# Kernel optimization log

Measured on AMD Instinct MI355X. Metric: run time of the kernel, lower is better.

The kernel has to match this reference:

```python
import jax, jax.numpy as jnp
import numpy as np

B, S, H = 64, 1024, 512
NEG = -1e10


def setup_inputs() -> dict:
    key = jax.random.key(0)
    ks = jax.random.split(key, 10)
    hidden = jax.random.normal(ks[0], (B, H), dtype=jnp.float32)
    encoder_outputs = jax.random.normal(ks[1], (S, B, H), dtype=jnp.float32)
    attn_mask = jax.random.randint(ks[2], (B, S), 0, 2, dtype=jnp.int32)
    src_gps_seqs = jax.random.uniform(ks[3], (S, B, 2), dtype=jnp.float32)
    src = jax.random.uniform(ks[4], (S, B, 3), dtype=jnp.float32)
    src_rids = jax.random.randint(ks[5], (S, B, 1), 0, 10000, dtype=jnp.int64)
    input_id = jax.random.randint(ks[6], (B, 1), 0, 10000, dtype=jnp.int64)
    trg_gps_seqs = jax.random.uniform(ks[7], (B, 2), dtype=jnp.float32)
    # learned params: attn = Linear(2H -> H), v = Linear(H -> 1, no bias)
    bound = 1.0 / np.sqrt(2 * H)
    attn_w = jax.random.uniform(ks[8], (H, 2 * H), minval=-bound, maxval=bound, dtype=jnp.float32)
    attn_b = jnp.zeros((H,), dtype=jnp.float32)
    v_w = jax.random.uniform(ks[9], (1, H), minval=-1.0 / np.sqrt(H), maxval=1.0 / np.sqrt(H), dtype=jnp.float32)
    return {"t": 0, "hidden": hidden, "encoder_outputs": encoder_outputs,
            "attn_mask": attn_mask, "src_gps_seqs": src_gps_seqs, "src": src,
            "src_rids": src_rids, "input_id": input_id, "trg_gps_seqs": trg_gps_seqs,
            "attn_w": attn_w, "attn_b": attn_b, "v_w": v_w}


def reference(t, hidden, encoder_outputs, attn_mask, src_gps_seqs, src,
              src_rids, input_id, trg_gps_seqs, attn_w, attn_b, v_w):
    # encoder_outputs: [S, B, H] -> [B, S, H]
    enc = jnp.transpose(encoder_outputs, (1, 0, 2))
    s_len = enc.shape[1]
    # hidden [B, H] broadcast over src_len -> [B, S, H]
    h = jnp.broadcast_to(hidden[:, None, :], (hidden.shape[0], s_len, hidden.shape[1]))
    cat = jnp.concatenate([h, enc], axis=2)                      # [B, S, 2H]
    energy = jnp.tanh(jnp.einsum('bsk,hk->bsh', cat, attn_w) + attn_b)  # [B, S, H]
    attention = jnp.einsum('bsh,oh->bs', energy, v_w)            # [B, S]
    attention = jnp.where(attn_mask == 0, jnp.float32(NEG), attention)
    return jax.nn.softmax(attention, axis=1)
```

## Files before the change

### kernel.cpp

```cpp
#include <hip/hip_runtime.h>
#include <hip/hip_bf16.h>

typedef unsigned short ushort_t;
typedef unsigned int uint_t;
typedef __attribute__((ext_vector_type(8))) short short8;
typedef __attribute__((ext_vector_type(4))) float f32x4;

#define NEG_VAL -1e10f

#define GL16(gp, lp) __builtin_amdgcn_global_load_lds( \
    (const __attribute__((address_space(1))) uint_t*)(gp), \
    (__attribute__((address_space(3))) uint_t*)(lp), 16, 0, 0)

__device__ __forceinline__ ushort_t f2bf(float x) {
    uint_t u = __float_as_uint(x);
    uint_t r = (u + 0x7fffu + ((u >> 16) & 1u)) >> 16;
    return (ushort_t)r;
}

__device__ __forceinline__ uint_t pkbf(float a, float b) {
    return (uint_t)f2bf(a) | ((uint_t)f2bf(b) << 16);
}

__device__ __forceinline__ uint_t cvtpk(float a, float b) {
    uint_t r;
    asm("v_cvt_pk_bf16_f32 %0, %1, %2" : "=v"(r) : "v"(a), "v"(b));
    return r;
}

__device__ __forceinline__ float tanh_fast(float x) {
    float e = __expf(2.0f * x);
    return 1.0f - 2.0f / (e + 1.0f);
}

__global__ void w2conv_kernel(const float* __restrict__ attn_w, ushort_t* __restrict__ w2) {
    int gid = blockIdx.x * 256 + threadIdx.x;
    int h = gid >> 7, q = gid & 127;
    float4 v = *(const float4*)(attn_w + (size_t)h * 1024 + 512 + q * 4);
    uint2 p;
    p.x = pkbf(v.x, v.y);
    p.y = pkbf(v.z, v.w);
    *(uint2*)(w2 + h * 512 + q * 4) = p;
}

__global__ void hproj_kernel(const float* __restrict__ hidden,
                             const float* __restrict__ attn_w,
                             const float* __restrict__ attn_b,
                             float* __restrict__ hb) {
    int gid = blockIdx.x * 256 + threadIdx.x;
    int b = gid >> 9, h = gid & 511;
    const float4* hp = (const float4*)(hidden + (size_t)b * 512);
    const float4* wp = (const float4*)(attn_w + (size_t)h * 1024);
    float a0 = 0.f, a1 = 0.f, a2 = 0.f, a3 = 0.f;
    #pragma unroll 4
    for (int i = 0; i < 128; i += 4) {
        float4 x0 = hp[i + 0], w0 = wp[i + 0];
        a0 += x0.x * w0.x + x0.y * w0.y + x0.z * w0.z + x0.w * w0.w;
        float4 x1 = hp[i + 1], w1 = wp[i + 1];
        a1 += x1.x * w1.x + x1.y * w1.y + x1.z * w1.z + x1.w * w1.w;
        float4 x2 = hp[i + 2], w2v = wp[i + 2];
        a2 += x2.x * w2v.x + x2.y * w2v.y + x2.z * w2v.z + x2.w * w2v.w;
        float4 x3 = hp[i + 3], w3 = wp[i + 3];
        a3 += x3.x * w3.x + x3.y * w3.y + x3.z * w3.z + x3.w * w3.w;
    }
    hb[gid] = attn_b[h] + ((a0 + a1) + (a2 + a3));
}

__global__ __launch_bounds__(256, 2) void gemm_kernel(
    const float* __restrict__ enc,
    const ushort_t* __restrict__ w2,
    const float* __restrict__ hb,
    const float* __restrict__ vw,
    float* __restrict__ part)
{
    __shared__ __align__(16) float As[2][128 * 32];
    __shared__ __align__(16) ushort_t Bs[2][256 * 32];
    __shared__ float red[2][128];

    const int tid = threadIdx.x;
    const int bid = blockIdx.x;
    const int xcd = bid & 7, j = bid >> 3;
    const int mt = xcd * 64 + (j >> 1), nt = j & 1;
    const size_t m0 = (size_t)mt * 128;
    const int h0 = nt * 256;

    const int wv = tid >> 6, l = tid & 63;
    const int wm = wv >> 1, wn = wv & 1;
    const int lr = l & 15, lq = l >> 4;

    const float* aG[4];
    uint_t aL[4];
    #pragma unroll
    for (int i = 0; i < 4; i++) {
        int rowA = i * 32 + wv * 8 + (l >> 3);
        int jA = (l & 7) ^ (l >> 3);
        aG[i] = enc + (m0 + rowA) * 512 + jA * 4;
        aL[i] = (uint_t)(i * 256 + wv * 64) * 16;
    }
    const ushort_t* bG[4];
    uint_t bL[4];
    #pragma unroll
    for (int i = 0; i < 4; i++) {
        int rowB = i * 64 + wv * 16 + (l >> 2);
        int jB = (l & 3) ^ ((l >> 3) & 3);
        bG[i] = w2 + (size_t)(h0 + rowB) * 512 + jB * 8;
        bL[i] = (uint_t)(i * 256 + wv * 64) * 16;
    }

    uint_t aoffL[4], aoffH[4], boff[8];
    #pragma unroll
    for (int mf = 0; mf < 4; mf++) {
        int row = wm * 64 + mf * 16 + lr;
        aoffL[mf] = (uint_t)row * 128 + (uint_t)(((lq * 2 + 0) ^ (row & 7)) * 16);
        aoffH[mf] = (uint_t)row * 128 + (uint_t)(((lq * 2 + 1) ^ (row & 7)) * 16);
    }
    #pragma unroll
    for (int nf = 0; nf < 8; nf++) {
        int r = wn * 128 + nf * 16 + lr;
        boff[nf] = (uint_t)r * 64 + (uint_t)((lq ^ ((r >> 1) & 3)) * 16);
    }

    #define STAGE(kt, buf) do { \
        _Pragma("unroll") \
        for (int i = 0; i < 4; i++) GL16(aG[i] + (kt) * 32, (char*)(&As[(buf)][0]) + aL[i]); \
        _Pragma("unroll") \
        for (int i = 0; i < 4; i++) GL16(bG[i] + (kt) * 32, (char*)(&Bs[(buf)][0]) + bL[i]); \
    } while (0)

    STAGE(0, 0);
    __syncthreads();

    f32x4 acc[4][8] = {};

    #pragma unroll 2
    for (int kt = 0; kt < 16; ++kt) {
        const int cur = kt & 1;
        if (kt < 15) STAGE(kt + 1, cur ^ 1);
        short8 af[4], bfr[8];
        #pragma unroll
        for (int nf = 0; nf < 8; nf++)
            bfr[nf] = *(const short8*)((const char*)(&Bs[cur][0]) + boff[nf]);
        #pragma unroll
        for (int mf = 0; mf < 4; mf++) {
            f32x4 lo = *(const f32x4*)((const char*)(&As[cur][0]) + aoffL[mf]);
            f32x4 hi = *(const f32x4*)((const char*)(&As[cur][0]) + aoffH[mf]);
            union { short8 s; uint_t u[4]; } t;
            t.u[0] = cvtpk(lo[0], lo[1]);
            t.u[1] = cvtpk(lo[2], lo[3]);
            t.u[2] = cvtpk(hi[0], hi[1]);
            t.u[3] = cvtpk(hi[2], hi[3]);
            af[mf] = t.s;
        }
        #pragma unroll
        for (int mf = 0; mf < 4; mf++)
            #pragma unroll
            for (int nf = 0; nf < 8; nf++)
                acc[mf][nf] = __builtin_amdgcn_mfma_f32_16x16x32_bf16(af[mf], bfr[nf], acc[mf][nf], 0, 0, 0);
        __syncthreads();
    }
    #undef STAGE

    float vv[8];
    #pragma unroll
    for (int nf = 0; nf < 8; nf++) vv[nf] = vw[h0 + wn * 128 + nf * 16 + lr];

    #pragma unroll
    for (int mf = 0; mf < 4; mf++) {
        #pragma unroll
        for (int r = 0; r < 4; r++) {
            int row = wm * 64 + mf * 16 + lq * 4 + r;
            int b = row & 63;
            const float* hbp = hb + b * 512 + h0 + wn * 128 + lr;
            float p = 0.f;
            #pragma unroll
            for (int nf = 0; nf < 8; nf++) {
                float x = acc[mf][nf][r] + hbp[nf * 16];
                p += tanh_fast(x) * vv[nf];
            }
            p += __shfl_xor(p, 1);
            p += __shfl_xor(p, 2);
            p += __shfl_xor(p, 4);
            p += __shfl_xor(p, 8);
            if (lr == 0) red[wn][row] = p;
        }
    }
    __syncthreads();
    if (tid < 128) {
        part[(size_t)nt * 65536 + m0 + tid] = red[0][tid] + red[1][tid];
    }
}

__global__ void softmax_kernel(const float* __restrict__ part,
                               const int* __restrict__ mask,
                               float* __restrict__ out) {
    __shared__ float sred[8];
    int b = blockIdx.x;
    int t = threadIdx.x;
    float vals[4];
    float mx = -INFINITY;
    #pragma unroll
    for (int i = 0; i < 4; i++) {
        int s = t + i * 256;
        int row = s * 64 + b;
        float x = part[row] + part[65536 + row];
        if (mask[b * 1024 + s] == 0) x = NEG_VAL;
        vals[i] = x;
        mx = fmaxf(mx, x);
    }
    #pragma unroll
    for (int o = 32; o; o >>= 1) mx = fmaxf(mx, __shfl_xor(mx, o));
    int w = t >> 6;
    if ((t & 63) == 0) sred[w] = mx;
    __syncthreads();
    mx = fmaxf(fmaxf(sred[0], sred[1]), fmaxf(sred[2], sred[3]));
    float sum = 0.f;
    #pragma unroll
    for (int i = 0; i < 4; i++) {
        vals[i] = __expf(vals[i] - mx);
        sum += vals[i];
    }
    #pragma unroll
    for (int o = 32; o; o >>= 1) sum += __shfl_xor(sum, o);
    if ((t & 63) == 0) sred[4 + w] = sum;
    __syncthreads();
    float tot = (sred[4] + sred[5]) + (sred[6] + sred[7]);
    float inv = 1.0f / tot;
    #pragma unroll
    for (int i = 0; i < 4; i++) out[b * 1024 + t + i * 256] = vals[i] * inv;
}

extern "C" void kernel_launch(void* const* d_in, const int* in_sizes, int n_in,
                              void* d_out, int out_size, void* d_ws, size_t ws_size,
                              hipStream_t stream) {
    const float* hidden = (const float*)d_in[1];
    const float* enc    = (const float*)d_in[2];
    const int*   mask   = (const int*)d_in[3];
    const float* attn_w = (const float*)d_in[9];
    const float* attn_b = (const float*)d_in[10];
    const float* vw     = (const float*)d_in[11];
    float* out = (float*)d_out;

    char* ws = (char*)d_ws;
    ushort_t* w2 = (ushort_t*)ws;
    float* hb   = (float*)(ws + 512 * 1024);
    float* part = (float*)(ws + 640 * 1024);

    w2conv_kernel<<<256, 256, 0, stream>>>(attn_w, w2);
    hproj_kernel<<<128, 256, 0, stream>>>(hidden, attn_w, attn_b, hb);
    gemm_kernel<<<1024, 256, 0, stream>>>(enc, w2, hb, vw, part);
    softmax_kernel<<<64, 256, 0, stream>>>(part, mask, out);
}
```

Measured before the change: 95.51 us.

## Enlarge GEMM tile to 256x256 with 512 threads and triple-buffered LDS pipeline

The encoder GEMM block grows to 256 rows and 8 waves, with a 2x4 wave grid. LDS moves to three-stage buffering, using explicit vmcnt waits and raw barriers instead of a full syncthreads per k-step. A and B staging are interleaved with split MFMA halves under raised wave priority. The aim is better latency hiding and more reuse of the B tile, at the cost of about 150 KB LDS per block, which limits occupancy to one block per CU.

```diff
diff --git a/kernel.cpp b/kernel.cpp
--- a/kernel.cpp
+++ b/kernel.cpp
@@ -66,84 +66,94 @@
     hb[gid] = attn_b[h] + ((a0 + a1) + (a2 + a3));
 }
 
-__global__ __launch_bounds__(256, 2) void gemm_kernel(
+__global__ __launch_bounds__(512, 2) void gemm_kernel(
     const float* __restrict__ enc,
     const ushort_t* __restrict__ w2,
     const float* __restrict__ hb,
     const float* __restrict__ vw,
     float* __restrict__ part)
 {
-    __shared__ __align__(16) float As[2][128 * 32];
-    __shared__ __align__(16) ushort_t Bs[2][256 * 32];
-    __shared__ float red[2][128];
+    __shared__ __align__(16) float As[3][256 * 32];
+    __shared__ __align__(16) ushort_t Bs[3][256 * 32];
+    __shared__ float red[4][256];
 
     const int tid = threadIdx.x;
     const int bid = blockIdx.x;
     const int xcd = bid & 7, j = bid >> 3;
-    const int mt = xcd * 64 + (j >> 1), nt = j & 1;
-    const size_t m0 = (size_t)mt * 128;
+    const int mt = xcd * 32 + (j >> 1), nt = j & 1;
+    const size_t m0 = (size_t)mt * 256;
     const int h0 = nt * 256;
 
     const int wv = tid >> 6, l = tid & 63;
-    const int wm = wv >> 1, wn = wv & 1;
+    const int wm = wv >> 2, wn = wv & 3;
     const int lr = l & 15, lq = l >> 4;
 
     const float* aG[4];
     uint_t aL[4];
     #pragma unroll
     for (int i = 0; i < 4; i++) {
-        int rowA = i * 32 + wv * 8 + (l >> 3);
-        int jA = (l & 7) ^ (l >> 3);
-        aG[i] = enc + (m0 + rowA) * 512 + jA * 4;
-        aL[i] = (uint_t)(i * 256 + wv * 64) * 16;
-    }
-    const ushort_t* bG[4];
-    uint_t bL[4];
-    #pragma unroll
-    for (int i = 0; i < 4; i++) {
-        int rowB = i * 64 + wv * 16 + (l >> 2);
-        int jB = (l & 3) ^ ((l >> 3) & 3);
-        bG[i] = w2 + (size_t)(h0 + rowB) * 512 + jB * 8;
-        bL[i] = (uint_t)(i * 256 + wv * 64) * 16;
-    }
-
-    uint_t aoffL[4], aoffH[4], boff[8];
-    #pragma unroll
-    for (int mf = 0; mf < 4; mf++) {
-        int row = wm * 64 + mf * 16 + lr;
-        aoffL[mf] = (uint_t)row * 128 + (uint_t)(((lq * 2 + 0) ^ (row & 7)) * 16);
-        aoffH[mf] = (uint_t)row * 128 + (uint_t)(((lq * 2 + 1) ^ (row & 7)) * 16);
-    }
-    #pragma unroll
-    for (int nf = 0; nf < 8; nf++) {
-        int r = wn * 128 + nf * 16 + lr;
+        int row = i * 64 + (tid >> 3);
+        int jj = (tid & 7) ^ ((tid >> 3) & 7);
+        aG[i] = enc + (m0 + row) * 512 + jj * 4;
+        aL[i] = (uint_t)(i * 512 + wv * 64) * 16;
+    }
+    const ushort_t* bG[2];
+    uint_t bL[2];
+    #pragma unroll
+    for (int i = 0; i < 2; i++) {
+        int row = i * 128 + (tid >> 2);
+        int jj = (tid & 3) ^ ((tid >> 3) & 3);
+        bG[i] = w2 + (size_t)(h0 + row) * 512 + jj * 8;
+        bL[i] = (uint_t)(i * 512 + wv * 64) * 16;
+    }
+
+    uint_t aoff0[8], aoff1[8], boff[4];
+    #pragma unroll
+    for (int mf = 0; mf < 8; mf++) {
+        int r = wm * 128 + mf * 16 + lr;
+        aoff0[mf] = (uint_t)r * 128 + (uint_t)(((lq * 2 + 0) ^ (r & 7)) * 16);
+        aoff1[mf] = (uint_t)r * 128 + (uint_t)(((lq * 2 + 1) ^ (r & 7)) * 16);
+    }
+    #pragma unroll
+    for (int nf = 0; nf < 4; nf++) {
+        int r = wn * 64 + nf * 16 + lr;
         boff[nf] = (uint_t)r * 64 + (uint_t)((lq ^ ((r >> 1) & 3)) * 16);
     }
 
-    #define STAGE(kt, buf) do { \
+    #define STAGE_A(kt, buf) do { \
         _Pragma("unroll") \
         for (int i = 0; i < 4; i++) GL16(aG[i] + (kt) * 32, (char*)(&As[(buf)][0]) + aL[i]); \
+    } while (0)
+    #define STAGE_B(kt, buf) do { \
         _Pragma("unroll") \
-        for (int i = 0; i < 4; i++) GL16(bG[i] + (kt) * 32, (char*)(&Bs[(buf)][0]) + bL[i]); \
+        for (int i = 0; i < 2; i++) GL16(bG[i] + (kt) * 32, (char*)(&Bs[(buf)][0]) + bL[i]); \
     } while (0)
 
-    STAGE(0, 0);
-    __syncthreads();
-
-    f32x4 acc[4][8] = {};
-
-    #pragma unroll 2
+    STAGE_A(0, 0); STAGE_B(0, 0);
+    STAGE_A(1, 1); STAGE_B(1, 1);
+
+    f32x4 acc[8][4] = {};
+
+    #pragma unroll
     for (int kt = 0; kt < 16; ++kt) {
-        const int cur = kt & 1;
-        if (kt < 15) STAGE(kt + 1, cur ^ 1);
-        short8 af[4], bfr[8];
-        #pragma unroll
-        for (int nf = 0; nf < 8; nf++)
+        const int cur = kt % 3;
+        if (kt < 15) { asm volatile("s_waitcnt vmcnt(6)" ::: "memory"); }
+        else         { asm volatile("s_waitcnt vmcnt(0)" ::: "memory"); }
+        __builtin_amdgcn_s_barrier();
+        asm volatile("" ::: "memory");
+
+        if (kt + 2 <= 15) STAGE_A(kt + 2, (kt + 2) % 3);
+
+        short8 bfr[4];
+        #pragma unroll
+        for (int nf = 0; nf < 4; nf++)
             bfr[nf] = *(const short8*)((const char*)(&Bs[cur][0]) + boff[nf]);
+
+        short8 af[4];
         #pragma unroll
         for (int mf = 0; mf < 4; mf++) {
-            f32x4 lo = *(const f32x4*)((const char*)(&As[cur][0]) + aoffL[mf]);
-            f32x4 hi = *(const f32x4*)((const char*)(&As[cur][0]) + aoffH[mf]);
+            f32x4 lo = *(const f32x4*)((const char*)(&As[cur][0]) + aoff0[mf]);
+            f32x4 hi = *(const f32x4*)((const char*)(&As[cur][0]) + aoff1[mf]);
             union { short8 s; uint_t u[4]; } t;
             t.u[0] = cvtpk(lo[0], lo[1]);
             t.u[1] = cvtpk(lo[2], lo[3]);
@@ -151,29 +161,53 @@
             t.u[3] = cvtpk(hi[2], hi[3]);
             af[mf] = t.s;
         }
+        __builtin_amdgcn_s_setprio(1);
         #pragma unroll
         for (int mf = 0; mf < 4; mf++)
             #pragma unroll
-            for (int nf = 0; nf < 8; nf++)
+            for (int nf = 0; nf < 4; nf++)
                 acc[mf][nf] = __builtin_amdgcn_mfma_f32_16x16x32_bf16(af[mf], bfr[nf], acc[mf][nf], 0, 0, 0);
-        __syncthreads();
-    }
-    #undef STAGE
-
-    float vv[8];
-    #pragma unroll
-    for (int nf = 0; nf < 8; nf++) vv[nf] = vw[h0 + wn * 128 + nf * 16 + lr];
-
-    #pragma unroll
-    for (int mf = 0; mf < 4; mf++) {
+        __builtin_amdgcn_s_setprio(0);
+
+        if (kt + 2 <= 15) STAGE_B(kt + 2, (kt + 2) % 3);
+
+        short8 ag[4];
+        #pragma unroll
+        for (int mf = 0; mf < 4; mf++) {
+            f32x4 lo = *(const f32x4*)((const char*)(&As[cur][0]) + aoff0[mf + 4]);
+            f32x4 hi = *(const f32x4*)((const char*)(&As[cur][0]) + aoff1[mf + 4]);
+            union { short8 s; uint_t u[4]; } t;
+            t.u[0] = cvtpk(lo[0], lo[1]);
+            t.u[1] = cvtpk(lo[2], lo[3]);
+            t.u[2] = cvtpk(hi[0], hi[1]);
+            t.u[3] = cvtpk(hi[2], hi[3]);
+            ag[mf] = t.s;
+        }
+        __builtin_amdgcn_s_setprio(1);
+        #pragma unroll
+        for (int mf = 0; mf < 4; mf++)
+            #pragma unroll
+            for (int nf = 0; nf < 4; nf++)
+                acc[mf + 4][nf] = __builtin_amdgcn_mfma_f32_16x16x32_bf16(ag[mf], bfr[nf], acc[mf + 4][nf], 0, 0, 0);
+        __builtin_amdgcn_s_setprio(0);
+    }
+    #undef STAGE_A
+    #undef STAGE_B
+
+    float vv[4];
+    #pragma unroll
+    for (int nf = 0; nf < 4; nf++) vv[nf] = vw[h0 + wn * 64 + nf * 16 + lr];
+
+    #pragma unroll
+    for (int mf = 0; mf < 8; mf++) {
         #pragma unroll
         for (int r = 0; r < 4; r++) {
-            int row = wm * 64 + mf * 16 + lq * 4 + r;
+            int row = wm * 128 + mf * 16 + lq * 4 + r;
             int b = row & 63;
-            const float* hbp = hb + b * 512 + h0 + wn * 128 + lr;
+            const float* hbp = hb + b * 512 + h0 + wn * 64 + lr;
             float p = 0.f;
             #pragma unroll
-            for (int nf = 0; nf < 8; nf++) {
+            for (int nf = 0; nf < 4; nf++) {
                 float x = acc[mf][nf][r] + hbp[nf * 16];
                 p += tanh_fast(x) * vv[nf];
             }
@@ -185,8 +219,9 @@
         }
     }
     __syncthreads();
-    if (tid < 128) {
-        part[(size_t)nt * 65536 + m0 + tid] = red[0][tid] + red[1][tid];
+    if (tid < 256) {
+        part[(size_t)nt * 65536 + m0 + tid] =
+            (red[0][tid] + red[1][tid]) + (red[2][tid] + red[3][tid]);
     }
 }
 
@@ -247,6 +282,6 @@
 
     w2conv_kernel<<<256, 256, 0, stream>>>(attn_w, w2);
     hproj_kernel<<<128, 256, 0, stream>>>(hidden, attn_w, attn_b, hb);
-    gemm_kernel<<<1024, 256, 0, stream>>>(enc, w2, hb, vw, part);
+    gemm_kernel<<<512, 512, 0, stream>>>(enc, w2, hb, vw, part);
     softmax_kernel<<<64, 256, 0, stream>>>(part, mask, out);
 }
```

Measured after the change: 102.6 us. +7.4%, slower.

## Split GEMM tile across eight waves with smaller per-wave output tiles

Applied to the files above, without the earlier changes.

Grows the GEMM block from 4 to 8 waves in a 2x4 wave grid, so each wave computes a 64x64 sub-tile instead of 64x128. This halves the accumulators per wave and simplifies the staging address math to two loads per operand per thread. The aim is to raise latency hiding and cut register pressure. The catch is that launch_bounds(512,4) caps registers tightly enough to cause spills. LDS use of about 64KB per block also keeps actual residency well below the requested bound.

```diff
diff --git a/kernel.cpp b/kernel.cpp
--- a/kernel.cpp
+++ b/kernel.cpp
@@ -66,7 +66,7 @@
     hb[gid] = attn_b[h] + ((a0 + a1) + (a2 + a3));
 }
 
-__global__ __launch_bounds__(256, 2) void gemm_kernel(
+__global__ __launch_bounds__(512, 4) void gemm_kernel(
     const float* __restrict__ enc,
     const ushort_t* __restrict__ w2,
     const float* __restrict__ hb,
@@ -75,7 +75,7 @@
 {
     __shared__ __align__(16) float As[2][128 * 32];
     __shared__ __align__(16) ushort_t Bs[2][256 * 32];
-    __shared__ float red[2][128];
+    __shared__ float red[4][128];
 
     const int tid = threadIdx.x;
     const int bid = blockIdx.x;
@@ -85,65 +85,44 @@
     const int h0 = nt * 256;
 
     const int wv = tid >> 6, l = tid & 63;
-    const int wm = wv >> 1, wn = wv & 1;
+    const int wm = wv >> 2, wn = wv & 3;
     const int lr = l & 15, lq = l >> 4;
 
-    const float* aG[4];
-    uint_t aL[4];
-    #pragma unroll
-    for (int i = 0; i < 4; i++) {
-        int rowA = i * 32 + wv * 8 + (l >> 3);
-        int jA = (l & 7) ^ (l >> 3);
-        aG[i] = enc + (m0 + rowA) * 512 + jA * 4;
-        aL[i] = (uint_t)(i * 256 + wv * 64) * 16;
-    }
-    const ushort_t* bG[4];
-    uint_t bL[4];
-    #pragma unroll
-    for (int i = 0; i < 4; i++) {
-        int rowB = i * 64 + wv * 16 + (l >> 2);
-        int jB = (l & 3) ^ ((l >> 3) & 3);
-        bG[i] = w2 + (size_t)(h0 + rowB) * 512 + jB * 8;
-        bL[i] = (uint_t)(i * 256 + wv * 64) * 16;
-    }
-
-    uint_t aoffL[4], aoffH[4], boff[8];
-    #pragma unroll
-    for (int mf = 0; mf < 4; mf++) {
-        int row = wm * 64 + mf * 16 + lr;
-        aoffL[mf] = (uint_t)row * 128 + (uint_t)(((lq * 2 + 0) ^ (row & 7)) * 16);
-        aoffH[mf] = (uint_t)row * 128 + (uint_t)(((lq * 2 + 1) ^ (row & 7)) * 16);
-    }
-    #pragma unroll
-    for (int nf = 0; nf < 8; nf++) {
-        int r = wn * 128 + nf * 16 + lr;
-        boff[nf] = (uint_t)r * 64 + (uint_t)((lq ^ ((r >> 1) & 3)) * 16);
-    }
+    const float* aG = enc + (m0 + (tid >> 3)) * 512 + (((tid & 7) ^ ((tid >> 3) & 7)) << 2);
+    const uint_t aLb = (uint_t)__builtin_amdgcn_readfirstlane(wv * 64) * 16;
+    const ushort_t* bG = w2 + (size_t)(h0 + (tid >> 2)) * 512 + (((tid & 3) ^ ((tid >> 3) & 3)) << 3);
+    const uint_t bLb = aLb;
+
+    const int ra = wm * 64 + lr;
+    const uint_t aoff0 = (uint_t)ra * 128 + (uint_t)(((lq * 2 + 0) ^ (ra & 7)) * 16);
+    const uint_t aoff1 = (uint_t)ra * 128 + (uint_t)(((lq * 2 + 1) ^ (ra & 7)) * 16);
+    const int rb = wn * 64 + lr;
+    const uint_t boff = (uint_t)rb * 64 + (uint_t)((lq ^ ((rb >> 1) & 3)) * 16);
 
     #define STAGE(kt, buf) do { \
-        _Pragma("unroll") \
-        for (int i = 0; i < 4; i++) GL16(aG[i] + (kt) * 32, (char*)(&As[(buf)][0]) + aL[i]); \
-        _Pragma("unroll") \
-        for (int i = 0; i < 4; i++) GL16(bG[i] + (kt) * 32, (char*)(&Bs[(buf)][0]) + bL[i]); \
+        GL16(aG + (kt) * 32,         (char*)(&As[(buf)][0]) + aLb); \
+        GL16(aG + (kt) * 32 + 32768, (char*)(&As[(buf)][0]) + aLb + 8192); \
+        GL16(bG + (kt) * 32,         (char*)(&Bs[(buf)][0]) + bLb); \
+        GL16(bG + (kt) * 32 + 65536, (char*)(&Bs[(buf)][0]) + bLb + 8192); \
     } while (0)
 
     STAGE(0, 0);
     __syncthreads();
 
-    f32x4 acc[4][8] = {};
+    f32x4 acc[4][4] = {};
 
     #pragma unroll 2
     for (int kt = 0; kt < 16; ++kt) {
         const int cur = kt & 1;
         if (kt < 15) STAGE(kt + 1, cur ^ 1);
-        short8 af[4], bfr[8];
-        #pragma unroll
-        for (int nf = 0; nf < 8; nf++)
-            bfr[nf] = *(const short8*)((const char*)(&Bs[cur][0]) + boff[nf]);
+        short8 af[4], bfr[4];
+        #pragma unroll
+        for (int nf = 0; nf < 4; nf++)
+            bfr[nf] = *(const short8*)((const char*)(&Bs[cur][0]) + boff + nf * 1024);
         #pragma unroll
         for (int mf = 0; mf < 4; mf++) {
-            f32x4 lo = *(const f32x4*)((const char*)(&As[cur][0]) + aoffL[mf]);
-            f32x4 hi = *(const f32x4*)((const char*)(&As[cur][0]) + aoffH[mf]);
+            f32x4 lo = *(const f32x4*)((const char*)(&As[cur][0]) + aoff0 + mf * 2048);
+            f32x4 hi = *(const f32x4*)((const char*)(&As[cur][0]) + aoff1 + mf * 2048);
             union { short8 s; uint_t u[4]; } t;
             t.u[0] = cvtpk(lo[0], lo[1]);
             t.u[1] = cvtpk(lo[2], lo[3]);
@@ -154,15 +133,15 @@
         #pragma unroll
         for (int mf = 0; mf < 4; mf++)
             #pragma unroll
-            for (int nf = 0; nf < 8; nf++)
+            for (int nf = 0; nf < 4; nf++)
                 acc[mf][nf] = __builtin_amdgcn_mfma_f32_16x16x32_bf16(af[mf], bfr[nf], acc[mf][nf], 0, 0, 0);
         __syncthreads();
     }
     #undef STAGE
 
-    float vv[8];
-    #pragma unroll
-    for (int nf = 0; nf < 8; nf++) vv[nf] = vw[h0 + wn * 128 + nf * 16 + lr];
+    float vv[4];
+    #pragma unroll
+    for (int nf = 0; nf < 4; nf++) vv[nf] = vw[h0 + wn * 64 + nf * 16 + lr];
 
     #pragma unroll
     for (int mf = 0; mf < 4; mf++) {
@@ -170,10 +149,10 @@
         for (int r = 0; r < 4; r++) {
             int row = wm * 64 + mf * 16 + lq * 4 + r;
             int b = row & 63;
-            const float* hbp = hb + b * 512 + h0 + wn * 128 + lr;
+            const float* hbp = hb + b * 512 + h0 + wn * 64 + lr;
             float p = 0.f;
             #pragma unroll
-            for (int nf = 0; nf < 8; nf++) {
+            for (int nf = 0; nf < 4; nf++) {
                 float x = acc[mf][nf][r] + hbp[nf * 16];
                 p += tanh_fast(x) * vv[nf];
             }
@@ -186,7 +165,8 @@
     }
     __syncthreads();
     if (tid < 128) {
-        part[(size_t)nt * 65536 + m0 + tid] = red[0][tid] + red[1][tid];
+        part[(size_t)nt * 65536 + m0 + tid] =
+            (red[0][tid] + red[1][tid]) + (red[2][tid] + red[3][tid]);
     }
 }
 
@@ -247,6 +227,6 @@
 
     w2conv_kernel<<<256, 256, 0, stream>>>(attn_w, w2);
     hproj_kernel<<<128, 256, 0, stream>>>(hidden, attn_w, attn_b, hb);
-    gemm_kernel<<<1024, 256, 0, stream>>>(enc, w2, hb, vw, part);
+    gemm_kernel<<<1024, 512, 0, stream>>>(enc, w2, hb, vw, part);
     softmax_kernel<<<64, 256, 0, stream>>>(part, mask, out);
 }
```

Result: faster. 93.45 us (-2.2%).
